# Kernel optimization log

Hardware: AMD Instinct MI355X
Metric: run time of the kernel (lower is better)

Reference implementation:

```python
import jax, jax.numpy as jnp
import numpy as np

DIM = 1024
HEADS = 16
HEAD_DIM = DIM // HEADS
EPS = 1e-5
THETA = 10000.0


def _rope(t):
    # t: (b, s, d). lucidrains rotary: interleaved pairs, full-dim rotation, theta=10000.
    b, s, d = t.shape
    inv_freq = 1.0 / (THETA ** (jnp.arange(0, d, 2, dtype=jnp.float32) / d))  # (d/2,)
    ang = jnp.arange(s, dtype=jnp.float32)[:, None] * inv_freq[None, :]        # (s, d/2)
    cos, sin = jnp.cos(ang), jnp.sin(ang)
    tp = t.reshape(b, s, d // 2, 2)
    x1, x2 = tp[..., 0], tp[..., 1]
    o1 = x1 * cos - x2 * sin
    o2 = x2 * cos + x1 * sin
    return jnp.stack([o1, o2], axis=-1).reshape(b, s, d)


def setup_inputs() -> dict:
    key = jax.random.key(0)
    ks = jax.random.split(key, 10)
    b, s, d = 2, 2048, DIM
    scale = 1.0 / np.sqrt(d)
    return {
        "x": jax.random.normal(ks[0], (b, s, d), dtype=jnp.float32),
        "mask": jax.random.normal(ks[1], (b, s, s), dtype=jnp.float32),
        "ln_g": jnp.ones((d,), dtype=jnp.float32),
        "ln_b": jnp.zeros((d,), dtype=jnp.float32),
        "w_qkv": jax.random.normal(ks[2], (3 * d, d), dtype=jnp.float32) * scale,
        "b_qkv": jnp.zeros((3 * d,), dtype=jnp.float32),
        "in_w": jax.random.normal(ks[3], (3 * d, d), dtype=jnp.float32) * scale,
        "in_b": jnp.zeros((3 * d,), dtype=jnp.float32),
        "out_w": jax.random.normal(ks[4], (d, d), dtype=jnp.float32) * scale,
        "out_b": jnp.zeros((d,), dtype=jnp.float32),
    }


def reference(x, mask, ln_g, ln_b, w_qkv, b_qkv, in_w, in_b, out_w, out_b):
    b, s, d = x.shape
    # LayerNorm
    mu = jnp.mean(x, axis=-1, keepdims=True)
    var = jnp.mean((x - mu) ** 2, axis=-1, keepdims=True)
    xn = (x - mu) * jax.lax.rsqrt(var + EPS) * ln_g + ln_b
    # fused qkv projection, then chunk
    qkv = xn @ w_qkv.T + b_qkv
    q, k, v = jnp.split(qkv, 3, axis=-1)
    # RoPE on q, k (full dim, interleaved pairs)
    q = _rope(q)
    k = _rope(k)
    # nn.MultiheadAttention re-applies its own in-projection
    wq, wk, wv = jnp.split(in_w, 3, axis=0)
    bq, bk, bv = jnp.split(in_b, 3, axis=0)
    def to_heads(t, w, bias):
        t = t @ w.T + bias
        return t.reshape(b, s, HEADS, HEAD_DIM).transpose(0, 2, 1, 3)  # (b,h,s,hd)
    qh = to_heads(q, wq, bq)
    kh = to_heads(k, wk, bk)
    vh = to_heads(v, wv, bv)
    scores = jnp.einsum('bhid,bhjd->bhij', qh, kh) / np.sqrt(HEAD_DIM)
    scores = scores + mask[:, None, :, :]  # mask repeated over heads
    attn = jax.nn.softmax(scores, axis=-1)
    out = jnp.einsum('bhij,bhjd->bhid', attn, vh)
    out = out.transpose(0, 2, 1, 3).reshape(b, s, d)
    return out @ out_w.T + out_b
```

## Files before the change

kernel.cpp:

```cpp
#include <hip/hip_runtime.h>

using u16 = unsigned short;
using u32 = unsigned int;
typedef __attribute__((ext_vector_type(8))) short short8;
typedef __attribute__((ext_vector_type(4))) float f32x4;

#define LOG2E 1.4426950408889634f
#define SCALE2 0.18033688011112042f

__device__ __forceinline__ u16 f2b(float f) {
  union { float f; unsigned u; } v; v.f = f;
  unsigned r = v.u + 0x7fffu + ((v.u >> 16) & 1u);
  return (u16)(r >> 16);
}

__device__ __forceinline__ void wg_barrier() {
  asm volatile("s_waitcnt lgkmcnt(0)\n\ts_barrier" ::: "memory");
}

__global__ __launch_bounds__(256) void prep(const float* __restrict__ w_qkv, u16* __restrict__ wqkv_b,
                                            const float* __restrict__ in_w, u16* __restrict__ inw_b,
                                            const float* __restrict__ out_w, u16* __restrict__ outw_b,
                                            float2* __restrict__ rtab,
                                            const float* __restrict__ mask, u16* __restrict__ maskp,
                                            const float* __restrict__ x,
                                            const float* __restrict__ ln_g,
                                            const float* __restrict__ ln_b,
                                            u16* __restrict__ xn) {
  __shared__ u16 T[128 * 68];
  __shared__ float sbuf[4], ssbuf[4];
  int blk = blockIdx.x, t = threadIdx.x;
  if (blk < 7168) {
    int i = blk * 256 + t;
    const float* s; u16* d; int off;
    if (i < 786432)       { s = w_qkv; d = wqkv_b; off = i; }
    else if (i < 1572864) { s = in_w;  d = inw_b;  off = i - 786432; }
    else                  { s = out_w; d = outw_b; off = i - 1572864; }
    float4 v = ((const float4*)s)[off];
    uint2 o;
    o.x = (unsigned)f2b(v.x) | ((unsigned)f2b(v.y) << 16);
    o.y = (unsigned)f2b(v.z) | ((unsigned)f2b(v.w) << 16);
    ((uint2*)d)[off] = o;
  } else if (blk < 11264) {
    int idx = (blk - 7168) * 256 + t;
    int pos = idx >> 9, i = idx & 511;
    float ifreq = exp2f(-(float)(2 * i) * (13.287712379549449f / 1024.0f));
    float ang = (float)pos * ifreq;
    rtab[idx] = make_float2(__cosf(ang), __sinf(ang));
  } else if (blk < 12288) {
    int mb = blk - 11264;
    int kt = mb & 31, qt = (mb >> 5) & 15, bb = mb >> 9;
    const float* src = mask + ((size_t)bb * 2048 + qt * 128) * 2048 + kt * 64;
    #pragma unroll
    for (int it = 0; it < 8; it++) {
      int id = it * 256 + t;
      int r = id >> 4, c4 = (id & 15) * 4;
      float4 v = *(const float4*)(src + (size_t)r * 2048 + c4);
      T[r * 68 + c4 + 0] = f2b(v.x * LOG2E);
      T[r * 68 + c4 + 1] = f2b(v.y * LOG2E);
      T[r * 68 + c4 + 2] = f2b(v.z * LOG2E);
      T[r * 68 + c4 + 3] = f2b(v.w * LOG2E);
    }
    __syncthreads();
    size_t obase = (size_t)(((bb * 16 + qt) * 32) + kt) * 8192;
    #pragma unroll
    for (int it = 0; it < 2; it++) {
      int pos = it * 256 + t;
      int l15 = pos & 15, g = pos >> 4;
      int w = g >> 3, p = (g >> 2) & 1, qd = g & 3;
      int qlocal = w * 32 + p * 16 + l15;
      u16 vals[16];
      #pragma unroll
      for (int mt = 0; mt < 4; mt++)
        #pragma unroll
        for (int reg = 0; reg < 4; reg++)
          vals[mt * 4 + reg] = T[qlocal * 68 + mt * 16 + qd * 4 + reg];
      uint4* dst = (uint4*)(maskp + obase + (size_t)pos * 16);
      dst[0] = *(uint4*)&vals[0];
      dst[1] = *(uint4*)&vals[8];
    }
  } else {
    int row = blk - 12288;
    const float* xr = x + (size_t)row * 1024;
    float4 v = *(const float4*)(xr + t * 4);
    float s = v.x + v.y + v.z + v.w;
    float ss = v.x * v.x + v.y * v.y + v.z * v.z + v.w * v.w;
    #pragma unroll
    for (int m = 1; m < 64; m <<= 1) {
      s  += __shfl_xor(s, m);
      ss += __shfl_xor(ss, m);
    }
    int wave = t >> 6, lane = t & 63;
    if (lane == 0) { sbuf[wave] = s; ssbuf[wave] = ss; }
    __syncthreads();
    s  = sbuf[0] + sbuf[1] + sbuf[2] + sbuf[3];
    ss = ssbuf[0] + ssbuf[1] + ssbuf[2] + ssbuf[3];
    float mean = s * (1.0f / 1024.0f);
    float var  = ss * (1.0f / 1024.0f) - mean * mean;
    float rstd = 1.0f / sqrtf(var + 1e-5f);
    float4 gv = *(const float4*)(ln_g + t * 4);
    float4 bv = *(const float4*)(ln_b + t * 4);
    uint2 o;
    o.x = (unsigned)f2b((v.x - mean) * rstd * gv.x + bv.x) |
          ((unsigned)f2b((v.y - mean) * rstd * gv.y + bv.y) << 16);
    o.y = (unsigned)f2b((v.z - mean) * rstd * gv.z + bv.z) |
          ((unsigned)f2b((v.w - mean) * rstd * gv.w + bv.w) << 16);
    *(uint2*)(xn + (size_t)row * 1024 + t * 4) = o;
  }
}

template<bool SLAB, bool OUT_BF16, bool ROPE, bool WVT>
__global__ __launch_bounds__(256, 3) void gemm_pipe(const u16* __restrict__ A, int lda,
                                                    const u16* __restrict__ W,
                                                    const float* __restrict__ bias,
                                                    const float2* __restrict__ rtab,
                                                    float* __restrict__ Cf,
                                                    u16* __restrict__ Cb,
                                                    u16* __restrict__ vT,
                                                    int ldc, int K) {
  __shared__ u16 As[2][128 * 36];
  __shared__ u16 Bs[2][128 * 36];
  int n0 = blockIdx.x * 128, m0 = blockIdx.y * 128;
  int aoff = SLAB ? ((n0 >> 10) << 10) : 0;
  int tid = threadIdx.x;
  int lane = tid & 63, l15 = lane & 15, quad = lane >> 4;
  int w = tid >> 6, mw = w & 1, nw = w >> 1;
  const u16* Abase = A + (size_t)m0 * lda + aoff;
  const u16* Wbase = W + (size_t)n0 * K;
  int r0 = tid >> 2;
  int c4 = (tid & 3) * 8;
  f32x4 acc[4][4];
  #pragma unroll
  for (int i = 0; i < 4; i++)
    #pragma unroll
    for (int j = 0; j < 4; j++) acc[i][j] = (f32x4){0.f, 0.f, 0.f, 0.f};

  uint4 a0, a1, w0, w1;
  uint4 b0, b1, x0, x1;
  #define GLOADS_A(k0)                                                        \
    a0 = *(const uint4*)(Abase + (size_t)(r0)      * lda + (k0) + c4);        \
    a1 = *(const uint4*)(Abase + (size_t)(r0 + 64) * lda + (k0) + c4);        \
    w0 = *(const uint4*)(Wbase + (size_t)(r0)      * K   + (k0) + c4);        \
    w1 = *(const uint4*)(Wbase + (size_t)(r0 + 64) * K   + (k0) + c4);
  #define GLOADS_B(k0)                                                        \
    b0 = *(const uint4*)(Abase + (size_t)(r0)      * lda + (k0) + c4);        \
    b1 = *(const uint4*)(Abase + (size_t)(r0 + 64) * lda + (k0) + c4);        \
    x0 = *(const uint4*)(Wbase + (size_t)(r0)      * K   + (k0) + c4);        \
    x1 = *(const uint4*)(Wbase + (size_t)(r0 + 64) * K   + (k0) + c4);
  #define LSTORES_A(bf)                                                       \
    *(uint4*)&As[bf][(r0)      * 36 + c4] = a0;                               \
    *(uint4*)&As[bf][(r0 + 64) * 36 + c4] = a1;                               \
    *(uint4*)&Bs[bf][(r0)      * 36 + c4] = w0;                               \
    *(uint4*)&Bs[bf][(r0 + 64) * 36 + c4] = w1;
  #define LSTORES_B(bf)                                                       \
    *(uint4*)&As[bf][(r0)      * 36 + c4] = b0;                               \
    *(uint4*)&As[bf][(r0 + 64) * 36 + c4] = b1;                               \
    *(uint4*)&Bs[bf][(r0)      * 36 + c4] = x0;                               \
    *(uint4*)&Bs[bf][(r0 + 64) * 36 + c4] = x1;
  #define COMPUTE(bf)                                                         \
    {                                                                         \
      short8 af[4], bfr[4];                                                   \
      _Pragma("unroll")                                                       \
      for (int mt = 0; mt < 4; mt++)                                          \
        af[mt] = *(const short8*)&As[bf][(mw * 64 + mt * 16 + l15) * 36 + quad * 8]; \
      _Pragma("unroll")                                                       \
      for (int nt = 0; nt < 4; nt++)                                          \
        bfr[nt] = *(const short8*)&Bs[bf][(nw * 64 + nt * 16 + l15) * 36 + quad * 8]; \
      _Pragma("unroll")                                                       \
      for (int mt = 0; mt < 4; mt++)                                          \
        _Pragma("unroll")                                                     \
        for (int nt = 0; nt < 4; nt++)                                        \
          acc[mt][nt] = __builtin_amdgcn_mfma_f32_16x16x32_bf16(              \
              af[mt], bfr[nt], acc[mt][nt], 0, 0, 0);                         \
    }

  GLOADS_A(0);
  LSTORES_A(0);
  GLOADS_A(32);
  GLOADS_B(64);
  wg_barrier();
  for (int k0 = 0; k0 < K; k0 += 64) {
    if (k0 + 32 < K)  { LSTORES_A(1); }
    if (k0 + 96 < K)  { GLOADS_A(k0 + 96); }
    COMPUTE(0);
    wg_barrier();
    if (k0 + 64 < K)  { LSTORES_B(0); }
    if (k0 + 128 < K) { GLOADS_B(k0 + 128); }
    COMPUTE(1);
    wg_barrier();
  }
  #undef GLOADS_A
  #undef GLOADS_B
  #undef LSTORES_A
  #undef LSTORES_B
  #undef COMPUTE
  int mb = m0 + mw * 64, nb = n0 + nw * 64;
  float bv[4];
  #pragma unroll
  for (int nt = 0; nt < 4; nt++) bv[nt] = bias[nb + nt * 16 + l15];
  #pragma unroll
  for (int mt = 0; mt < 4; mt++)
    #pragma unroll
    for (int nt = 0; nt < 4; nt++) {
      int col = nb + nt * 16 + l15;
      if (WVT && col >= 2048) {
        int hh = (col - 2048) >> 6, dd = (col - 2048) & 63;
        int row0 = mb + mt * 16 + quad * 4;
        int bbi = row0 >> 11, s0 = row0 & 2047;
        u16 vv[4];
        #pragma unroll
        for (int reg = 0; reg < 4; reg++) vv[reg] = f2b(acc[mt][nt][reg] + bv[nt]);
        *(uint2*)&vT[((size_t)((bbi * 16 + hh) * 64 + dd)) * 2048 + s0] = *(uint2*)vv;
      } else {
        #pragma unroll
        for (int reg = 0; reg < 4; reg++) {
          int row = mb + mt * 16 + quad * 4 + reg;
          float val = acc[mt][nt][reg] + bv[nt];
          if (ROPE && col < 2048) {
            float pr = __shfl_xor(val, 1);
            float2 cs = rtab[(size_t)(row & 2047) * 512 + ((col & 1023) >> 1)];
            val = (col & 1) ? fmaf(val, cs.x, pr * cs.y)
                            : fmaf(val, cs.x, -pr * cs.y);
          }
          if (OUT_BF16) Cb[(size_t)row * ldc + col] = f2b(val);
          else          Cf[(size_t)row * ldc + col] = val;
        }
      }
    }
}

__global__ __launch_bounds__(512, 4) void attn_mfma(const u16* __restrict__ qkv2,
                                                    const u16* __restrict__ vT,
                                                    const u16* __restrict__ maskp,
                                                    u16* __restrict__ attn_out) {
  __shared__ u16 Kb[2][64 * 72];
  __shared__ u16 Vb[2][64 * 72];
  __shared__ u16 Ps[128 * 72];
  int h = blockIdx.x, qt = blockIdx.y, bb = blockIdx.z;
  int tid = threadIdx.x;
  int lane = tid & 63, l15 = lane & 15, quad = lane >> 4;
  int w = tid >> 6;
  int sr = tid >> 3, sc = (tid & 7) * 8;
  const u16* kslab = qkv2 + ((size_t)bb * 2048) * 3072 + 1024 + h * 64;
  const u16* vslab = vT + ((size_t)((bb * 16 + h) * 64)) * 2048;

  {
    int r = tid >> 2, c0 = (tid & 3) * 16;
    const u16* src = qkv2 + (size_t)(bb * 2048 + qt * 128 + r) * 3072 + h * 64 + c0;
    *(uint4*)&Ps[r * 72 + c0]     = *(const uint4*)src;
    *(uint4*)&Ps[r * 72 + c0 + 8] = *(const uint4*)(src + 8);
  }
  {
    *(uint4*)&Kb[0][sr * 72 + sc] = *(const uint4*)(kslab + (size_t)sr * 3072 + sc);
    *(uint4*)&Vb[0][sr * 72 + sc] = *(const uint4*)(vslab + (size_t)sr * 2048 + sc);
  }
  short8 bq[2];
  #pragma unroll
  for (int hk = 0; hk < 2; hk++)
    bq[hk] = *(const short8*)&Ps[(w * 16 + l15) * 72 + hk * 32 + quad * 8];
  float lsum = 0.f;
  f32x4 acc[4];
  #pragma unroll
  for (int dt = 0; dt < 4; dt++) acc[dt] = (f32x4){0.f, 0.f, 0.f, 0.f};
  const u16* mtile = maskp + ((size_t)((bb * 16 + qt) * 32)) * 8192
                     + ((w * 4 + quad) * 16 + l15) * 16;
  uint4 mA, mB;
  {
    const uint4* mq = (const uint4*)mtile;
    mA = mq[0]; mB = mq[1];
  }
  wg_barrier();

  for (int kt = 0; kt < 32; kt++) {
    int b = kt & 1;
    uint4 kr, vr, mAn, mBn;
    if (kt + 1 < 32) {
      kr = *(const uint4*)(kslab + (size_t)((kt + 1) * 64 + sr) * 3072 + sc);
      vr = *(const uint4*)(vslab + (size_t)sr * 2048 + (kt + 1) * 64 + sc);
      const uint4* mq = (const uint4*)(mtile + (size_t)(kt + 1) * 8192);
      mAn = mq[0]; mBn = mq[1];
    }
    short8 ak[4][2];
    #pragma unroll
    for (int mt = 0; mt < 4; mt++)
      #pragma unroll
      for (int hk = 0; hk < 2; hk++)
        ak[mt][hk] = *(const short8*)&Kb[b][(mt * 16 + l15) * 72 + hk * 32 + quad * 8];
    f32x4 st[4];
    #pragma unroll
    for (int mt = 0; mt < 4; mt++) {
      f32x4 z = (f32x4){0.f, 0.f, 0.f, 0.f};
      z = __builtin_amdgcn_mfma_f32_16x16x32_bf16(ak[mt][0], bq[0], z, 0, 0, 0);
      st[mt] = __builtin_amdgcn_mfma_f32_16x16x32_bf16(ak[mt][1], bq[1], st[mt] = z, 0, 0, 0);
    }
    u32 wds[8] = {mA.x, mA.y, mA.z, mA.w, mB.x, mB.y, mB.z, mB.w};
    float mv[16];
    #pragma unroll
    for (int j = 0; j < 8; j++) {
      mv[2 * j]     = __uint_as_float(wds[j] << 16);
      mv[2 * j + 1] = __uint_as_float(wds[j] & 0xffff0000u);
    }
    int prow = (w * 16 + l15) * 72 + quad * 4;
    #pragma unroll
    for (int mt = 0; mt < 4; mt++) {
      float sv0 = fmaf(st[mt][0], SCALE2, mv[mt * 4 + 0]);
      float sv1 = fmaf(st[mt][1], SCALE2, mv[mt * 4 + 1]);
      float sv2 = fmaf(st[mt][2], SCALE2, mv[mt * 4 + 2]);
      float sv3 = fmaf(st[mt][3], SCALE2, mv[mt * 4 + 3]);
      float p0 = __builtin_amdgcn_exp2f(sv0), p1 = __builtin_amdgcn_exp2f(sv1);
      float p2 = __builtin_amdgcn_exp2f(sv2), p3 = __builtin_amdgcn_exp2f(sv3);
      lsum += (p0 + p1) + (p2 + p3);
      u32 pk0, pk1;
      asm("v_cvt_pk_bf16_f32 %0, %1, %2" : "=v"(pk0) : "v"(p0), "v"(p1));
      asm("v_cvt_pk_bf16_f32 %0, %1, %2" : "=v"(pk1) : "v"(p2), "v"(p3));
      *(uint2*)&Ps[prow + mt * 16] = make_uint2(pk0, pk1);
    }
    short8 ap[2];
    #pragma unroll
    for (int hk = 0; hk < 2; hk++)
      ap[hk] = *(const short8*)&Ps[(w * 16 + l15) * 72 + hk * 32 + quad * 8];
    #pragma unroll
    for (int dt = 0; dt < 4; dt++) {
      short8 bv0 = *(const short8*)&Vb[b][(dt * 16 + l15) * 72 + quad * 8];
      short8 bv1 = *(const short8*)&Vb[b][(dt * 16 + l15) * 72 + 32 + quad * 8];
      acc[dt] = __builtin_amdgcn_mfma_f32_16x16x32_bf16(ap[0], bv0, acc[dt], 0, 0, 0);
      acc[dt] = __builtin_amdgcn_mfma_f32_16x16x32_bf16(ap[1], bv1, acc[dt], 0, 0, 0);
    }
    if (kt + 1 < 32) {
      int nb = b ^ 1;
      *(uint4*)&Kb[nb][sr * 72 + sc] = kr;
      *(uint4*)&Vb[nb][sr * 72 + sc] = vr;
      mA = mAn; mB = mBn;
    }
    wg_barrier();
  }
  {
    float l = lsum;
    l += __shfl_xor(l, 16);
    l += __shfl_xor(l, 32);
    #pragma unroll
    for (int reg = 0; reg < 4; reg++) {
      float lq = __shfl(l, quad * 4 + reg);
      float inv = 1.0f / lq;
      int grow = bb * 2048 + qt * 128 + w * 16 + quad * 4 + reg;
      #pragma unroll
      for (int dt = 0; dt < 4; dt++)
        attn_out[(size_t)grow * 1024 + h * 64 + dt * 16 + l15] = f2b(acc[dt][reg] * inv);
    }
  }
}

extern "C" void kernel_launch(void* const* d_in, const int* in_sizes, int n_in,
                              void* d_out, int out_size, void* d_ws, size_t ws_size,
                              hipStream_t stream) {
  const float* x     = (const float*)d_in[0];
  const float* mask  = (const float*)d_in[1];
  const float* ln_g  = (const float*)d_in[2];
  const float* ln_b  = (const float*)d_in[3];
  const float* w_qkv = (const float*)d_in[4];
  const float* b_qkv = (const float*)d_in[5];
  const float* in_w  = (const float*)d_in[6];
  const float* in_b  = (const float*)d_in[7];
  const float* out_w = (const float*)d_in[8];
  const float* out_b = (const float*)d_in[9];
  float* out = (float*)d_out;
  char* ws = (char*)d_ws;

  u16* wqkv_b = (u16*)(ws);
  u16* inw_b  = (u16*)(ws + 6291456ull);
  u16* outw_b = (u16*)(ws + 12582912ull);
  u16* xn_b   = (u16*)(ws + 14680064ull);
  u16* attn_b = xn_b;
  u16* qkv_b  = (u16*)(ws + 23068672ull);
  u16* qkv2_b = (u16*)(ws + 48234496ull);
  float2* rtab = (float2*)qkv2_b;
  u16* vT     = (u16*)(ws + 73400320ull);
  u16* maskp  = (u16*)(ws + 81788928ull);

  prep<<<16384, 256, 0, stream>>>(w_qkv, wqkv_b, in_w, inw_b, out_w, outw_b,
                                  rtab, mask, maskp, x, ln_g, ln_b, xn_b);
  gemm_pipe<false, true, true, false><<<dim3(24, 32), 256, 0, stream>>>(
      xn_b, 1024, wqkv_b, b_qkv, rtab, nullptr, qkv_b, nullptr, 3072, 1024);
  gemm_pipe<true, true, false, true><<<dim3(24, 32), 256, 0, stream>>>(
      qkv_b, 3072, inw_b, in_b, nullptr, nullptr, qkv2_b, vT, 3072, 1024);
  attn_mfma<<<dim3(16, 16, 2), 512, 0, stream>>>(qkv2_b, vT, maskp, attn_b);
  gemm_pipe<false, false, false, false><<<dim3(8, 32), 256, 0, stream>>>(
      attn_b, 1024, outw_b, out_b, nullptr, out, nullptr, nullptr, 1024, 1024);
}
```

Baseline: 303.4 us.

## Split attention warps into 4x2 query/key grid with cross-warp reduction

Reassigns the 8 warps of the attention kernel from 8 query strips of 16 rows each to a 4x2 grid. Each warp now covers 32 query rows and half of each 64-key tile. Each V fragment loaded from LDS is reused across two query sub-tiles, and each warp loads fewer K fragments. Partial output accumulators and row sums from the two key halves are combined at the end through shared memory, which adds an extra barrier and reduction. The cost is more accumulator registers per warp, with some risk of register pressure under the 512-thread, 4-block launch bound.

```diff
diff --git a/kernel.cpp b/kernel.cpp
--- a/kernel.cpp
+++ b/kernel.cpp
@@ -236,10 +236,12 @@
   __shared__ u16 Kb[2][64 * 72];
   __shared__ u16 Vb[2][64 * 72];
   __shared__ u16 Ps[128 * 72];
+  __shared__ float lsf[128];
   int h = blockIdx.x, qt = blockIdx.y, bb = blockIdx.z;
   int tid = threadIdx.x;
   int lane = tid & 63, l15 = lane & 15, quad = lane >> 4;
   int w = tid >> 6;
+  int wq = w & 3, wk = w >> 2;
   int sr = tid >> 3, sc = (tid & 7) * 8;
   const u16* kslab = qkv2 + ((size_t)bb * 2048) * 3072 + 1024 + h * 64;
   const u16* vslab = vT + ((size_t)((bb * 16 + h) * 64)) * 2048;
@@ -254,98 +256,129 @@
     *(uint4*)&Kb[0][sr * 72 + sc] = *(const uint4*)(kslab + (size_t)sr * 3072 + sc);
     *(uint4*)&Vb[0][sr * 72 + sc] = *(const uint4*)(vslab + (size_t)sr * 2048 + sc);
   }
-  short8 bq[2];
+  const u16* mbase = maskp + ((size_t)((bb * 16 + qt) * 32)) * 8192
+                     + ((wq * 8 + quad) * 16 + l15) * 16 + wk * 8;
+  uint4 m0 = *(const uint4*)mbase;
+  uint4 m1 = *(const uint4*)(mbase + 1024);
+  wg_barrier();
+
+  short8 bq[2][2];
   #pragma unroll
-  for (int hk = 0; hk < 2; hk++)
-    bq[hk] = *(const short8*)&Ps[(w * 16 + l15) * 72 + hk * 32 + quad * 8];
-  float lsum = 0.f;
-  f32x4 acc[4];
+  for (int p = 0; p < 2; p++)
+    #pragma unroll
+    for (int hk = 0; hk < 2; hk++)
+      bq[p][hk] = *(const short8*)&Ps[(wq * 32 + p * 16 + l15) * 72 + hk * 32 + quad * 8];
+  float lsum[2] = {0.f, 0.f};
+  f32x4 acc[2][4];
   #pragma unroll
-  for (int dt = 0; dt < 4; dt++) acc[dt] = (f32x4){0.f, 0.f, 0.f, 0.f};
-  const u16* mtile = maskp + ((size_t)((bb * 16 + qt) * 32)) * 8192
-                     + ((w * 4 + quad) * 16 + l15) * 16;
-  uint4 mA, mB;
-  {
-    const uint4* mq = (const uint4*)mtile;
-    mA = mq[0]; mB = mq[1];
-  }
-  wg_barrier();
+  for (int p = 0; p < 2; p++)
+    #pragma unroll
+    for (int dt = 0; dt < 4; dt++) acc[p][dt] = (f32x4){0.f, 0.f, 0.f, 0.f};
 
   for (int kt = 0; kt < 32; kt++) {
     int b = kt & 1;
-    uint4 kr, vr, mAn, mBn;
+    uint4 kr, vr, m0n, m1n;
     if (kt + 1 < 32) {
       kr = *(const uint4*)(kslab + (size_t)((kt + 1) * 64 + sr) * 3072 + sc);
       vr = *(const uint4*)(vslab + (size_t)sr * 2048 + (kt + 1) * 64 + sc);
-      const uint4* mq = (const uint4*)(mtile + (size_t)(kt + 1) * 8192);
-      mAn = mq[0]; mBn = mq[1];
-    }
-    short8 ak[4][2];
-    #pragma unroll
-    for (int mt = 0; mt < 4; mt++)
+      m0n = *(const uint4*)(mbase + (size_t)(kt + 1) * 8192);
+      m1n = *(const uint4*)(mbase + (size_t)(kt + 1) * 8192 + 1024);
+    }
+    short8 ak[2][2];
+    #pragma unroll
+    for (int mt = 0; mt < 2; mt++)
       #pragma unroll
       for (int hk = 0; hk < 2; hk++)
-        ak[mt][hk] = *(const short8*)&Kb[b][(mt * 16 + l15) * 72 + hk * 32 + quad * 8];
-    f32x4 st[4];
-    #pragma unroll
-    for (int mt = 0; mt < 4; mt++) {
-      f32x4 z = (f32x4){0.f, 0.f, 0.f, 0.f};
-      z = __builtin_amdgcn_mfma_f32_16x16x32_bf16(ak[mt][0], bq[0], z, 0, 0, 0);
-      st[mt] = __builtin_amdgcn_mfma_f32_16x16x32_bf16(ak[mt][1], bq[1], st[mt] = z, 0, 0, 0);
-    }
-    u32 wds[8] = {mA.x, mA.y, mA.z, mA.w, mB.x, mB.y, mB.z, mB.w};
-    float mv[16];
-    #pragma unroll
-    for (int j = 0; j < 8; j++) {
-      mv[2 * j]     = __uint_as_float(wds[j] << 16);
-      mv[2 * j + 1] = __uint_as_float(wds[j] & 0xffff0000u);
-    }
-    int prow = (w * 16 + l15) * 72 + quad * 4;
-    #pragma unroll
-    for (int mt = 0; mt < 4; mt++) {
-      float sv0 = fmaf(st[mt][0], SCALE2, mv[mt * 4 + 0]);
-      float sv1 = fmaf(st[mt][1], SCALE2, mv[mt * 4 + 1]);
-      float sv2 = fmaf(st[mt][2], SCALE2, mv[mt * 4 + 2]);
-      float sv3 = fmaf(st[mt][3], SCALE2, mv[mt * 4 + 3]);
-      float p0 = __builtin_amdgcn_exp2f(sv0), p1 = __builtin_amdgcn_exp2f(sv1);
-      float p2 = __builtin_amdgcn_exp2f(sv2), p3 = __builtin_amdgcn_exp2f(sv3);
-      lsum += (p0 + p1) + (p2 + p3);
-      u32 pk0, pk1;
-      asm("v_cvt_pk_bf16_f32 %0, %1, %2" : "=v"(pk0) : "v"(p0), "v"(p1));
-      asm("v_cvt_pk_bf16_f32 %0, %1, %2" : "=v"(pk1) : "v"(p2), "v"(p3));
-      *(uint2*)&Ps[prow + mt * 16] = make_uint2(pk0, pk1);
+        ak[mt][hk] = *(const short8*)&Kb[b][(wk * 32 + mt * 16 + l15) * 72 + hk * 32 + quad * 8];
+    f32x4 st[2][2];
+    #pragma unroll
+    for (int p = 0; p < 2; p++)
+      #pragma unroll
+      for (int mt = 0; mt < 2; mt++) {
+        f32x4 z = (f32x4){0.f, 0.f, 0.f, 0.f};
+        z = __builtin_amdgcn_mfma_f32_16x16x32_bf16(ak[mt][0], bq[p][0], z, 0, 0, 0);
+        st[p][mt] = __builtin_amdgcn_mfma_f32_16x16x32_bf16(ak[mt][1], bq[p][1], z, 0, 0, 0);
+      }
+    #pragma unroll
+    for (int p = 0; p < 2; p++) {
+      uint4 mm = p ? m1 : m0;
+      u32 wds[4] = {mm.x, mm.y, mm.z, mm.w};
+      float mv[8];
+      #pragma unroll
+      for (int j = 0; j < 4; j++) {
+        mv[2 * j]     = __uint_as_float(wds[j] << 16);
+        mv[2 * j + 1] = __uint_as_float(wds[j] & 0xffff0000u);
+      }
+      int prow = (wq * 32 + p * 16 + l15) * 72 + wk * 32 + quad * 4;
+      #pragma unroll
+      for (int mt = 0; mt < 2; mt++) {
+        float sv0 = fmaf(st[p][mt][0], SCALE2, mv[mt * 4 + 0]);
+        float sv1 = fmaf(st[p][mt][1], SCALE2, mv[mt * 4 + 1]);
+        float sv2 = fmaf(st[p][mt][2], SCALE2, mv[mt * 4 + 2]);
+        float sv3 = fmaf(st[p][mt][3], SCALE2, mv[mt * 4 + 3]);
+        float p0 = __builtin_amdgcn_exp2f(sv0), p1 = __builtin_amdgcn_exp2f(sv1);
+        float p2 = __builtin_amdgcn_exp2f(sv2), p3 = __builtin_amdgcn_exp2f(sv3);
+        lsum[p] += (p0 + p1) + (p2 + p3);
+        u32 pk0, pk1;
+        asm("v_cvt_pk_bf16_f32 %0, %1, %2" : "=v"(pk0) : "v"(p0), "v"(p1));
+        asm("v_cvt_pk_bf16_f32 %0, %1, %2" : "=v"(pk1) : "v"(p2), "v"(p3));
+        *(uint2*)&Ps[prow + mt * 16] = make_uint2(pk0, pk1);
+      }
     }
     short8 ap[2];
     #pragma unroll
-    for (int hk = 0; hk < 2; hk++)
-      ap[hk] = *(const short8*)&Ps[(w * 16 + l15) * 72 + hk * 32 + quad * 8];
+    for (int p = 0; p < 2; p++)
+      ap[p] = *(const short8*)&Ps[(wq * 32 + p * 16 + l15) * 72 + wk * 32 + quad * 8];
     #pragma unroll
     for (int dt = 0; dt < 4; dt++) {
-      short8 bv0 = *(const short8*)&Vb[b][(dt * 16 + l15) * 72 + quad * 8];
-      short8 bv1 = *(const short8*)&Vb[b][(dt * 16 + l15) * 72 + 32 + quad * 8];
-      acc[dt] = __builtin_amdgcn_mfma_f32_16x16x32_bf16(ap[0], bv0, acc[dt], 0, 0, 0);
-      acc[dt] = __builtin_amdgcn_mfma_f32_16x16x32_bf16(ap[1], bv1, acc[dt], 0, 0, 0);
+      short8 bv = *(const short8*)&Vb[b][(dt * 16 + l15) * 72 + wk * 32 + quad * 8];
+      #pragma unroll
+      for (int p = 0; p < 2; p++)
+        acc[p][dt] = __builtin_amdgcn_mfma_f32_16x16x32_bf16(ap[p], bv, acc[p][dt], 0, 0, 0);
     }
     if (kt + 1 < 32) {
       int nb = b ^ 1;
       *(uint4*)&Kb[nb][sr * 72 + sc] = kr;
       *(uint4*)&Vb[nb][sr * 72 + sc] = vr;
-      mA = mAn; mB = mBn;
+      m0 = m0n; m1 = m1n;
     }
     wg_barrier();
   }
-  {
-    float l = lsum;
-    l += __shfl_xor(l, 16);
-    l += __shfl_xor(l, 32);
-    #pragma unroll
-    for (int reg = 0; reg < 4; reg++) {
-      float lq = __shfl(l, quad * 4 + reg);
-      float inv = 1.0f / lq;
-      int grow = bb * 2048 + qt * 128 + w * 16 + quad * 4 + reg;
+
+  float* fs = ((wq < 2) ? (float*)&Kb[0][0] : (float*)&Vb[0][0]) + (wq & 1) * 2176;
+  if (wk) {
+    #pragma unroll
+    for (int p = 0; p < 2; p++) {
       #pragma unroll
       for (int dt = 0; dt < 4; dt++)
-        attn_out[(size_t)grow * 1024 + h * 64 + dt * 16 + l15] = f2b(acc[dt][reg] * inv);
+        #pragma unroll
+        for (int reg = 0; reg < 4; reg++)
+          fs[(p * 16 + quad * 4 + reg) * 68 + dt * 16 + l15] = acc[p][dt][reg];
+      float l = lsum[p];
+      l += __shfl_xor(l, 16);
+      l += __shfl_xor(l, 32);
+      if (lane < 16) lsf[(wq * 2 + p) * 16 + l15] = l;
+    }
+  }
+  wg_barrier();
+  if (!wk) {
+    #pragma unroll
+    for (int p = 0; p < 2; p++) {
+      float l = lsum[p];
+      l += __shfl_xor(l, 16);
+      l += __shfl_xor(l, 32);
+      l += lsf[(wq * 2 + p) * 16 + l15];
+      #pragma unroll
+      for (int reg = 0; reg < 4; reg++) {
+        float lq = __shfl(l, quad * 4 + reg);
+        float inv = 1.0f / lq;
+        int grow = bb * 2048 + qt * 128 + wq * 32 + p * 16 + quad * 4 + reg;
+        #pragma unroll
+        for (int dt = 0; dt < 4; dt++) {
+          float o = acc[p][dt][reg] + fs[(p * 16 + quad * 4 + reg) * 68 + dt * 16 + l15];
+          attn_out[(size_t)grow * 1024 + h * 64 + dt * 16 + l15] = f2b(o * inv);
+        }
+      }
     }
   }
 }
```

Result: faster. 291.0 us (-4.1%).
